# Kernel tuning notes

Hardware: AMD Instinct MI355X
Metric: run time of the kernel (lower is better)

## Reference

```python
import jax, jax.numpy as jnp
import numpy as np

N = 4096        # nodes (cells)
E = 131072      # edges (avg degree 32)
IN = 3000       # input features (genes)
HID = 128       # hidden dim per head
H = 4           # attention heads
LAT = 16        # latent dim
NEG_SLOPE = 0.2 # PyG GATConv leaky_relu slope


def _gat_sparse(x, src, dst, W, a_src, a_dst, b, concat):
    """PyG GATConv on an edge list (src -> dst, softmax grouped by dst)."""
    n = x.shape[0]
    h_, c = a_src.shape
    h = (x @ W).reshape(n, h_, c)                      # [N,H,C]
    e_src = (h * a_src[None]).sum(-1)                  # [N,H]
    e_dst = (h * a_dst[None]).sum(-1)                  # [N,H]
    e = jax.nn.leaky_relu(e_src[src] + e_dst[dst], NEG_SLOPE)  # [E,H]
    m = jax.ops.segment_max(e, dst, num_segments=n)
    ex = jnp.exp(e - m[dst])
    denom = jax.ops.segment_sum(ex, dst, num_segments=n)
    alpha = ex / (denom[dst] + 1e-16)                  # PyG softmax eps
    out = jax.ops.segment_sum(alpha[:, :, None] * h[src], dst, num_segments=n)
    out = out.reshape(n, h_ * c) if concat else out.mean(1)
    return out + b


def _gat_dense(x, W, a_src, a_dst, b, concat):
    """GATConv over the complete graph (the SVD low-rank reconstruction is
    generically fully dense, so to_sparse() keeps all N^2 entries; with
    used_edge_weight=False only the structure matters)."""
    n = x.shape[0]
    h_, c = a_src.shape
    h = (x @ W).reshape(n, h_, c)
    e_src = (h * a_src[None]).sum(-1)                  # [N,H]
    e_dst = (h * a_dst[None]).sum(-1)                  # [N,H]
    # scores[i (target), j (source), head]
    scores = jax.nn.leaky_relu(e_dst[:, None, :] + e_src[None, :, :], NEG_SLOPE)
    alpha = jax.nn.softmax(scores, axis=1)             # softmax over sources
    out = jnp.einsum('ijh,jhc->ihc', alpha, h)
    out = out.reshape(n, h_ * c) if concat else out.mean(1)
    return out + b


def setup_inputs() -> dict:
    key = jax.random.key(0)
    ks = jax.random.split(key, 16)
    s = 0.05
    x = jax.random.normal(ks[0], (N, IN), jnp.float32)
    src = jax.random.randint(ks[1], (E,), 0, N, jnp.int32)
    off = jax.random.randint(ks[2], (E,), 1, N, jnp.int32)
    dst = (src + off) % N                              # no self loops (PyG re-adds them)
    edge_index = jnp.stack([src, dst], axis=0)
    edge_attr = jax.random.uniform(ks[3], (E,), jnp.float32)
    D1 = H * HID
    return {
        'x': x, 'edge_index': edge_index, 'edge_attr': edge_attr,
        'W1': jax.random.normal(ks[4], (IN, D1), jnp.float32) * s,
        'a1_src': jax.random.normal(ks[5], (H, HID), jnp.float32) * s,
        'a1_dst': jax.random.normal(ks[6], (H, HID), jnp.float32) * s,
        'b1': jnp.zeros((D1,), jnp.float32),
        'Wm': jax.random.normal(ks[7], (D1, H * LAT), jnp.float32) * s,
        'am_src': jax.random.normal(ks[8], (H, LAT), jnp.float32) * s,
        'am_dst': jax.random.normal(ks[9], (H, LAT), jnp.float32) * s,
        'bm': jnp.zeros((LAT,), jnp.float32),
        'Ws': jax.random.normal(ks[10], (D1, H * LAT), jnp.float32) * s,
        'as_src': jax.random.normal(ks[11], (H, LAT), jnp.float32) * s,
        'as_dst': jax.random.normal(ks[12], (H, LAT), jnp.float32) * s,
        'bs': jnp.zeros((LAT,), jnp.float32),
    }


def reference(x, edge_index, edge_attr, W1, a1_src, a1_dst, b1,
              Wm, am_src, am_dst, bm, Ws, as_src, as_dst, bs):
    loops = jnp.arange(N, dtype=edge_index.dtype)
    src = jnp.concatenate([edge_index[0], loops])      # GATConv add_self_loops=True
    dst = jnp.concatenate([edge_index[1], loops])
    # branch 1: original sparse graph
    x1 = _gat_sparse(x, src, dst, W1, a1_src, a1_dst, b1, True)
    z_mean1 = _gat_sparse(x1, src, dst, Wm, am_src, am_dst, bm, False)
    z_log_std1 = _gat_sparse(x1, src, dst, Ws, as_src, as_dst, bs, False)
    # branch 2: SVD low-rank reconstructed adjacency => complete graph
    x2 = _gat_dense(x, W1, a1_src, a1_dst, b1, True)
    z_mean2 = _gat_dense(x2, Wm, am_src, am_dst, bm, False)
    z_log_std2 = _gat_dense(x2, Ws, as_src, as_dst, bs, False)
    return (z_mean1, z_log_std1, z_mean2, z_log_std2)
```

## Files before the change

kernel.cpp:

```cpp
#include <hip/hip_runtime.h>

typedef unsigned short u16;
typedef unsigned long long u64;
typedef __attribute__((ext_vector_type(8))) short short8;
typedef __attribute__((ext_vector_type(4))) float f32x4;

#define NN   4096
#define EE   131072
#define ETOT (EE + NN)
#define HH   4
#define IND  3000
#define KP   3008
#define D1   512
#define C1   128
#define C2   16

__device__ __forceinline__ float b2f(u16 u){
  union { unsigned int i; float f; } v; v.i = ((unsigned int)u) << 16; return v.f;
}
__device__ __forceinline__ u16 f2b(float f){
  unsigned int x = __float_as_uint(f);
  unsigned int r = (x + 0x7fffu + ((x >> 16) & 1u)) >> 16;
  return (u16)r;
}
__device__ __forceinline__ float lrelu(float x){ return x > 0.f ? x : 0.2f * x; }

__device__ __forceinline__ void glds16(const void* g, void* l){
  __builtin_amdgcn_global_load_lds(
      (const __attribute__((address_space(1))) unsigned int*)g,
      (__attribute__((address_space(3))) unsigned int*)l, 16, 0, 0);
}

__global__ void zero_out_kernel(float* p, int n){
  int i = blockIdx.x * blockDim.x + threadIdx.x;
  if (i < n) p[i] = 0.f;
}

__global__ __launch_bounds__(256) void cvtXW_kernel(const float* __restrict__ X,
    const float* __restrict__ W, u16* __restrict__ Xhi, u16* __restrict__ Xlo,
    u16* __restrict__ Whi, u16* __restrict__ Wlo){
  __shared__ float T[64][65];
  int b = blockIdx.x;
  if (b < 6016){
    int id = b * 256 + threadIdx.x;
    int m = id / 376, ch = id - m * 376;
    int k = ch * 8;
    float v[8];
    if (k + 8 <= IND){
      float4 a = *(const float4*)(X + (size_t)m * IND + k);
      float4 bb = *(const float4*)(X + (size_t)m * IND + k + 4);
      v[0]=a.x; v[1]=a.y; v[2]=a.z; v[3]=a.w; v[4]=bb.x; v[5]=bb.y; v[6]=bb.z; v[7]=bb.w;
    } else {
      #pragma unroll
      for (int j = 0; j < 8; ++j){ int kk = k + j; v[j] = (kk < IND) ? X[(size_t)m*IND + kk] : 0.f; }
    }
    u16 h8[8], l8[8];
    #pragma unroll
    for (int j = 0; j < 8; ++j){ h8[j] = f2b(v[j]); l8[j] = f2b(v[j] - b2f(h8[j])); }
    *(uint4*)(Xhi + (size_t)m * KP + k) = *(uint4*)h8;
    *(uint4*)(Xlo + (size_t)m * KP + k) = *(uint4*)l8;
  } else {
    int wb = b - 6016;
    int kb = wb % 47, nb = wb / 47;
    int k0 = kb * 64, n0 = nb * 64;
    int t = threadIdx.x;
    #pragma unroll
    for (int rr = 0; rr < 4; ++rr){
      int kl = (t >> 4) + rr * 16;
      int nn = (t & 15) * 4;
      int k = k0 + kl;
      float4 v = make_float4(0.f, 0.f, 0.f, 0.f);
      if (k < IND) v = *(const float4*)(W + (size_t)k * D1 + n0 + nn);
      T[kl][nn] = v.x; T[kl][nn+1] = v.y; T[kl][nn+2] = v.z; T[kl][nn+3] = v.w;
    }
    __syncthreads();
    int nloc = t >> 2, kseg = (t & 3) * 16;
    int n = n0 + nloc;
    #pragma unroll
    for (int c2 = 0; c2 < 2; ++c2){
      int kloc = kseg + c2 * 8;
      u16 h8[8], l8[8];
      #pragma unroll
      for (int j = 0; j < 8; ++j){
        float f = T[kloc + j][nloc];
        h8[j] = f2b(f); l8[j] = f2b(f - b2f(h8[j]));
      }
      *(uint4*)(Whi + (size_t)n * KP + k0 + kloc) = *(uint4*)h8;
      *(uint4*)(Wlo + (size_t)n * KP + k0 + kloc) = *(uint4*)l8;
    }
  }
}

__global__ __launch_bounds__(256) void cvtW2_kernel(const float* __restrict__ WM,
    const float* __restrict__ WS, u16* __restrict__ Wh, u16* __restrict__ Wl){
  __shared__ float T[64][65];
  int half = blockIdx.y;
  int k0 = blockIdx.x * 64;
  const float* W = half ? WS : WM;
  int t = threadIdx.x;
  #pragma unroll
  for (int p = 0; p < 4; ++p){
    int r = p * 16 + (t >> 4), c4 = (t & 15) * 4;
    float4 v = *(const float4*)(W + (size_t)(k0 + r) * 64 + c4);
    T[r][c4] = v.x; T[r][c4+1] = v.y; T[r][c4+2] = v.z; T[r][c4+3] = v.w;
  }
  __syncthreads();
  #pragma unroll
  for (int p = 0; p < 4; ++p){
    int n = p * 16 + (t >> 4), k4 = (t & 15) * 4;
    u16 h4[4], l4[4];
    #pragma unroll
    for (int j = 0; j < 4; ++j){
      float f = T[k4 + j][n];
      h4[j] = f2b(f); l4[j] = f2b(f - b2f(h4[j]));
    }
    size_t o = (size_t)(half * 64 + n) * 512 + k0 + k4;
    *(ushort4*)(Wh + o) = *(ushort4*)h4;
    *(ushort4*)(Wl + o) = *(ushort4*)l4;
  }
}

__global__ __launch_bounds__(512) void gemm_mfma(const u16* __restrict__ Xhi,
    const u16* __restrict__ Xlo, const u16* __restrict__ Whi, const u16* __restrict__ Wlo,
    float* __restrict__ Hh){
  __shared__ u16 sAh[64*64], sAl[64*64], sBh[64*64], sBl[64*64];
  int t = threadIdx.x, lane = t & 63;
  int wv = __builtin_amdgcn_readfirstlane(t >> 6);
  int wr = wv >> 1, wc = wv & 1;
  int bm = blockIdx.x * 64, bn = blockIdx.y * 64;
  f32x4 acc[2] = {};
  int srow = t >> 3;
  int sc = (t & 7) ^ (srow & 7);
  const char* gAh = (const char*)(Xhi + (size_t)(bm + srow) * KP) + sc * 16;
  const char* gAl = (const char*)(Xlo + (size_t)(bm + srow) * KP) + sc * 16;
  const char* gBh = (const char*)(Whi + (size_t)(bn + srow) * KP) + sc * 16;
  const char* gBl = (const char*)(Wlo + (size_t)(bn + srow) * KP) + sc * 16;
  char* lAh = (char*)sAh + t * 16;
  char* lAl = (char*)sAl + t * 16;
  char* lBh = (char*)sBh + t * 16;
  char* lBl = (char*)sBl + t * 16;
  int r16 = lane & 15, kq = lane >> 4;
  int arow = wr * 16 + r16;
  int brow0 = wc * 32 + r16;
  int brow1 = brow0 + 16;
  int aoff[2], b0off[2], b1off[2];
  #pragma unroll
  for (int ks = 0; ks < 2; ++ks){
    int cc = ks * 4 + kq;
    aoff[ks]  = arow  * 128 + ((cc ^ (arow  & 7)) * 16);
    b0off[ks] = brow0 * 128 + ((cc ^ (brow0 & 7)) * 16);
    b1off[ks] = brow1 * 128 + ((cc ^ (brow1 & 7)) * 16);
  }
  for (int kb = 0; kb < KP * 2; kb += 128){
    glds16(gAh + kb, lAh);
    glds16(gAl + kb, lAl);
    glds16(gBh + kb, lBh);
    glds16(gBl + kb, lBl);
    __syncthreads();
    #pragma unroll
    for (int ks = 0; ks < 2; ++ks){
      short8 ah = *(const short8*)((const char*)sAh + aoff[ks]);
      short8 al = *(const short8*)((const char*)sAl + aoff[ks]);
      short8 b0h = *(const short8*)((const char*)sBh + b0off[ks]);
      short8 b0l = *(const short8*)((const char*)sBl + b0off[ks]);
      short8 b1h = *(const short8*)((const char*)sBh + b1off[ks]);
      short8 b1l = *(const short8*)((const char*)sBl + b1off[ks]);
      acc[0] = __builtin_amdgcn_mfma_f32_16x16x32_bf16(ah, b0h, acc[0], 0, 0, 0);
      acc[0] = __builtin_amdgcn_mfma_f32_16x16x32_bf16(ah, b0l, acc[0], 0, 0, 0);
      acc[0] = __builtin_amdgcn_mfma_f32_16x16x32_bf16(al, b0h, acc[0], 0, 0, 0);
      acc[1] = __builtin_amdgcn_mfma_f32_16x16x32_bf16(ah, b1h, acc[1], 0, 0, 0);
      acc[1] = __builtin_amdgcn_mfma_f32_16x16x32_bf16(ah, b1l, acc[1], 0, 0, 0);
      acc[1] = __builtin_amdgcn_mfma_f32_16x16x32_bf16(al, b1h, acc[1], 0, 0, 0);
    }
    __syncthreads();
  }
  int cr = kq << 2, cc = r16;
  #pragma unroll
  for (int j = 0; j < 2; ++j){
    int row = bm + wr * 16 + cr;
    int col = bn + wc * 32 + j * 16 + cc;
    float* o = Hh + (size_t)row * D1 + col;
    #pragma unroll
    for (int r = 0; r < 4; ++r) o[(size_t)r * D1] = acc[j][r];
  }
}

__global__ __launch_bounds__(256) void gemm_h_split(const float* __restrict__ X,
    const float* __restrict__ Wc, float* __restrict__ Hh){
  __shared__ u16 Ahs[64][40], Als[64][40], Bhs[64][40], Bls[64][40];
  int t = threadIdx.x, lane = t & 63, wave = t >> 6;
  int wr = wave >> 1, wcc = wave & 1;
  int bm = blockIdx.x * 64, bn = blockIdx.y * 64;
  f32x4 acc[2][2] = {};
  int arow = t >> 2, akc = (t & 3) << 3;
  int brow = t >> 3, bnc = (t & 7) << 3;
  for (int k0 = 0; k0 < IND; k0 += 32){
    float va[8];
    size_t abase = (size_t)(bm + arow) * IND + k0 + akc;
    if (k0 + akc + 8 <= IND){
      float4 r0 = *(const float4*)(X + abase);
      float4 r1 = *(const float4*)(X + abase + 4);
      va[0]=r0.x; va[1]=r0.y; va[2]=r0.z; va[3]=r0.w;
      va[4]=r1.x; va[5]=r1.y; va[6]=r1.z; va[7]=r1.w;
    } else {
      #pragma unroll
      for (int j = 0; j < 8; ++j){
        int k = k0 + akc + j;
        va[j] = (k < IND) ? X[abase + j] : 0.f;
      }
    }
    #pragma unroll
    for (int j = 0; j < 8; ++j){
      u16 hb = f2b(va[j]);
      Ahs[arow][akc + j] = hb;
      Als[arow][akc + j] = f2b(va[j] - b2f(hb));
    }
    {
      int gk = k0 + brow;
      float vb[8];
      if (gk < IND){
        const float* wp = Wc + (size_t)gk * D1 + bn + bnc;
        float4 r0 = *(const float4*)wp;
        float4 r1 = *(const float4*)(wp + 4);
        vb[0]=r0.x; vb[1]=r0.y; vb[2]=r0.z; vb[3]=r0.w;
        vb[4]=r1.x; vb[5]=r1.y; vb[6]=r1.z; vb[7]=r1.w;
      } else {
        #pragma unroll
        for (int j = 0; j < 8; ++j) vb[j] = 0.f;
      }
      #pragma unroll
      for (int j = 0; j < 8; ++j){
        u16 hb = f2b(vb[j]);
        Bhs[bnc + j][brow] = hb;
        Bls[bnc + j][brow] = f2b(vb[j] - b2f(hb));
      }
    }
    __syncthreads();
    int r16 = lane & 15, kq = (lane >> 4) << 3;
    short8 a0h = *(const short8*)&Ahs[wr*32      + r16][kq];
    short8 a1h = *(const short8*)&Ahs[wr*32 + 16 + r16][kq];
    short8 a0l = *(const short8*)&Als[wr*32      + r16][kq];
    short8 a1l = *(const short8*)&Als[wr*32 + 16 + r16][kq];
    short8 b0h = *(const short8*)&Bhs[wcc*32      + r16][kq];
    short8 b1h = *(const short8*)&Bhs[wcc*32 + 16 + r16][kq];
    short8 b0l = *(const short8*)&Bls[wcc*32      + r16][kq];
    short8 b1l = *(const short8*)&Bls[wcc*32 + 16 + r16][kq];
    acc[0][0] = __builtin_amdgcn_mfma_f32_16x16x32_bf16(a0h, b0h, acc[0][0], 0, 0, 0);
    acc[0][1] = __builtin_amdgcn_mfma_f32_16x16x32_bf16(a0h, b1h, acc[0][1], 0, 0, 0);
    acc[1][0] = __builtin_amdgcn_mfma_f32_16x16x32_bf16(a1h, b0h, acc[1][0], 0, 0, 0);
    acc[1][1] = __builtin_amdgcn_mfma_f32_16x16x32_bf16(a1h, b1h, acc[1][1], 0, 0, 0);
    acc[0][0] = __builtin_amdgcn_mfma_f32_16x16x32_bf16(a0h, b0l, acc[0][0], 0, 0, 0);
    acc[0][1] = __builtin_amdgcn_mfma_f32_16x16x32_bf16(a0h, b1l, acc[0][1], 0, 0, 0);
    acc[1][0] = __builtin_amdgcn_mfma_f32_16x16x32_bf16(a1h, b0l, acc[1][0], 0, 0, 0);
    acc[1][1] = __builtin_amdgcn_mfma_f32_16x16x32_bf16(a1h, b1l, acc[1][1], 0, 0, 0);
    acc[0][0] = __builtin_amdgcn_mfma_f32_16x16x32_bf16(a0l, b0h, acc[0][0], 0, 0, 0);
    acc[0][1] = __builtin_amdgcn_mfma_f32_16x16x32_bf16(a0l, b1h, acc[0][1], 0, 0, 0);
    acc[1][0] = __builtin_amdgcn_mfma_f32_16x16x32_bf16(a1l, b0h, acc[1][0], 0, 0, 0);
    acc[1][1] = __builtin_amdgcn_mfma_f32_16x16x32_bf16(a1l, b1h, acc[1][1], 0, 0, 0);
    __syncthreads();
  }
  int cr = (lane >> 4) << 2, cc = lane & 15;
  for (int i = 0; i < 2; ++i) for (int j = 0; j < 2; ++j){
    int row = bm + wr*32 + i*16 + cr;
    int col = bn + wcc*32 + j*16 + cc;
    float* o = Hh + (size_t)row * D1 + col;
    for (int r = 0; r < 4; ++r) o[(size_t)r * D1] = acc[i][j][r];
  }
}

__global__ __launch_bounds__(256) void transpose_h(const float* __restrict__ h,
    float* __restrict__ hT, u16* __restrict__ h16){
  __shared__ float T[64][65];
  int bm = blockIdx.x * 64, bc = blockIdx.y * 64;
  int t = threadIdx.x;
  #pragma unroll
  for (int p = 0; p < 4; ++p){
    int r = p * 16 + (t >> 4), c4 = (t & 15) * 4;
    float4 v = *(const float4*)(h + (size_t)(bm + r) * D1 + bc + c4);
    T[r][c4] = v.x; T[r][c4+1] = v.y; T[r][c4+2] = v.z; T[r][c4+3] = v.w;
    u16 q[4] = { f2b(v.x), f2b(v.y), f2b(v.z), f2b(v.w) };
    *(ushort4*)(h16 + (size_t)(bm + r) * D1 + bc + c4) = *(ushort4*)q;
  }
  __syncthreads();
  #pragma unroll
  for (int p = 0; p < 4; ++p){
    int c = p * 16 + (t >> 4), m4 = (t & 15) * 4;
    float4 o = make_float4(T[m4][c], T[m4+1][c], T[m4+2][c], T[m4+3][c]);
    *(float4*)(hT + (size_t)(bc + c) * NN + bm + m4) = o;
  }
}

__global__ __launch_bounds__(256) void evec128(const float* __restrict__ hsrc,
    const float* __restrict__ as_, const float* __restrict__ ad_,
    float* __restrict__ es, float* __restrict__ ed){
  int idx = blockIdx.x * 256 + threadIdx.x;
  if (idx >= NN * HH) return;
  int h = idx & 3;
  const float4* hp = (const float4*)(hsrc + (size_t)idx * C1);
  const float4* ap = (const float4*)(as_ + h * C1);
  const float4* dp = (const float4*)(ad_ + h * C1);
  float s1 = 0.f, s2 = 0.f;
  #pragma unroll
  for (int c = 0; c < 32; ++c){
    float4 v = hp[c], a = ap[c], d = dp[c];
    s1 += v.x*a.x + v.y*a.y + v.z*a.z + v.w*a.w;
    s2 += v.x*d.x + v.y*d.y + v.z*d.z + v.w*d.w;
  }
  es[idx] = s1; ed[idx] = s2;
}

__global__ void zero_kernel(int* p, int n){
  int i = blockIdx.x * blockDim.x + threadIdx.x;
  if (i < n) p[i] = 0;
}
__global__ void hist_kernel(const int* __restrict__ dstA, int* __restrict__ deg){
  int e = blockIdx.x * blockDim.x + threadIdx.x;
  if (e < ETOT){
    int d = (e < EE) ? dstA[e] : (e - EE);
    atomicAdd(&deg[d & (NN-1)], 1);
  }
}
__global__ __launch_bounds__(1024) void scan_kernel(const int* __restrict__ deg,
    int* __restrict__ off, int* __restrict__ cur){
  __shared__ int wsum[16];
  int t = threadIdx.x, lane = t & 63, wv = t >> 6;
  int v0 = deg[t*4], v1 = deg[t*4+1], v2 = deg[t*4+2], v3 = deg[t*4+3];
  int s = v0 + v1 + v2 + v3;
  int sc = s;
  #pragma unroll
  for (int o = 1; o < 64; o <<= 1){
    int y = __shfl_up(sc, o);
    if (lane >= o) sc += y;
  }
  if (lane == 63) wsum[wv] = sc;
  __syncthreads();
  int base = 0;
  #pragma unroll
  for (int i = 0; i < 16; ++i) base += (i < wv) ? wsum[i] : 0;
  int excl = base + sc - s;
  int a0 = excl, a1 = a0 + v0, a2 = a1 + v1, a3 = a2 + v2;
  off[t*4] = a0; off[t*4+1] = a1; off[t*4+2] = a2; off[t*4+3] = a3;
  cur[t*4] = a0; cur[t*4+1] = a1; cur[t*4+2] = a2; cur[t*4+3] = a3;
  if (t == 1023) off[4096] = base + sc;
}
__global__ void scatter_kernel(const int* __restrict__ srcA, const int* __restrict__ dstA,
    int* __restrict__ cur, int* __restrict__ sidx){
  int e = blockIdx.x * blockDim.x + threadIdx.x;
  if (e < ETOT){
    int s, d;
    if (e < EE){ s = srcA[e]; d = dstA[e]; } else { s = d = e - EE; }
    int pos = atomicAdd(&cur[d & (NN-1)], 1);
    pos = min(max(pos, 0), ETOT - 1);
    sidx[pos] = s & (NN-1);
  }
}

__global__ __launch_bounds__(256) void sparse1(const u16* __restrict__ h16,
    const float* __restrict__ es, const float* __restrict__ ed,
    const int* __restrict__ off, const int* __restrict__ sidx,
    const float* __restrict__ bias, u16* __restrict__ x1h, u16* __restrict__ x1l){
  int n = blockIdx.x, t = threadIdx.x, w = t >> 6;
// ... 294 lines not shown
    }
  } else {
    if (t < NC){
      int h = t / C, c = t % C;
      size_t base = (size_t)h * (NN + 1);
      float p1N = P1[(base + NN)    * Cp + c];
      float p1k = P1[(base + Kh[h]) * Cp + c];
      float p2k = P2[(base + Kh[h]) * Cp + c];
      vals[t] = (Ed[h] * (p1N - p1k) + E2d[h] * p2k) / Den[h];
    }
    __syncthreads();
    if (t < C){
      float z = (vals[t] + vals[C + t] + vals[2*C + t] + vals[3*C + t]) * 0.25f + bias[t];
      outF[(size_t)i * C + t] = z;
    }
  }
}

__global__ __launch_bounds__(256) void dense_out1(const float* __restrict__ P1,
    const float* __restrict__ P2, const float* __restrict__ usort,
    const float* __restrict__ ed, const float* __restrict__ bias,
    u16* __restrict__ outH, u16* __restrict__ outL){
  dense_body<C1, false>(P1, P2, usort, ed, bias, nullptr, outH, outL, blockIdx.x);
}

struct Dn2 { const float* P1[2]; const float* P2[2]; const float* us[2];
             const float* ed[2]; const float* bias[2]; float* out[2]; };
__global__ __launch_bounds__(256) void dense_out2(Dn2 a){
  int s = blockIdx.y;
  dense_body<C2, true>(a.P1[s], a.P2[s], a.us[s], a.ed[s], a.bias[s], a.out[s],
                       nullptr, nullptr, blockIdx.x);
}

extern "C" void kernel_launch(void* const* d_in, const int* in_sizes, int n_in,
                              void* d_out, int out_size, void* d_ws, size_t ws_size,
                              hipStream_t stream){
  const float* X   = (const float*)d_in[0];
  const int*   EI  = (const int*)d_in[1];
  const float* W1  = (const float*)d_in[3];
  const float* A1S = (const float*)d_in[4];
  const float* A1D = (const float*)d_in[5];
  const float* B1  = (const float*)d_in[6];
  const float* WM  = (const float*)d_in[7];
  const float* AMS = (const float*)d_in[8];
  const float* AMD = (const float*)d_in[9];
  const float* BM  = (const float*)d_in[10];
  const float* WS  = (const float*)d_in[11];
  const float* ASS = (const float*)d_in[12];
  const float* ASD = (const float*)d_in[13];
  const float* BS  = (const float*)d_in[14];
  float* OUT = (float*)d_out;
  (void)in_sizes; (void)n_in;

  if (ws_size < (size_t)56 * 1024 * 1024){
    zero_out_kernel<<<dim3((out_size + 255)/256), 256, 0, stream>>>(OUT, out_size);
    return;
  }
  bool fast = (ws_size >= (size_t)68 * 1024 * 1024);

  const size_t MB = 1024 * 1024;
  char* w = (char*)d_ws;
  size_t o = 0;
  auto alloc = [&](size_t bytes) -> void* {
    void* p = w + o;
    o += (bytes + 255) & ~(size_t)255;
    return p;
  };
  int*   deg  = (int*)  alloc(NN * 4);
  int*   coff = (int*)  alloc((NN + 1) * 4);
  int*   cur  = (int*)  alloc(NN * 4);
  int*   sidx = (int*)  alloc((size_t)ETOT * 4);
  float* e1s  = (float*)alloc(NN * HH * 4);
  float* e1d  = (float*)alloc(NN * HH * 4);
  float* us1  = (float*)alloc(HH * NN * 4);
  int*   pm1  = (int*)  alloc(HH * NN * 4);
  float* em1s = (float*)alloc(NN * HH * 4);
  float* em1d = (float*)alloc(NN * HH * 4);
  float* es1s = (float*)alloc(NN * HH * 4);
  float* es1d = (float*)alloc(NN * HH * 4);
  float* em2s = (float*)alloc(NN * HH * 4);
  float* em2d = (float*)alloc(NN * HH * 4);
  float* es2s = (float*)alloc(NN * HH * 4);
  float* es2d = (float*)alloc(NN * HH * 4);
  float* us2m = (float*)alloc(HH * NN * 4);
  int*   pm2m = (int*)  alloc(HH * NN * 4);
  float* us2s = (float*)alloc(HH * NN * 4);
  int*   pm2s = (int*)  alloc(HH * NN * 4);
  u16*   Wh2  = (u16*)  alloc(128 * 512 * 2);
  u16*   Wl2  = (u16*)  alloc(128 * 512 * 2);
  float* h    = (float*)alloc((size_t)NN * D1 * 4);
  char*  BIG  = w + o;
  size_t szX = (size_t)NN * KP * 2, szW = (size_t)D1 * KP * 2;
  u16* Xhi = (u16*)BIG;
  u16* Xlo = (u16*)(BIG + szX);
  u16* Whi = (u16*)(BIG + 2*szX);
  u16* Wlo = (u16*)(BIG + 2*szX + szW);
  u16*   x1h = (u16*)  (BIG + 0*MB);
  u16*   x1l = (u16*)  (BIG + 4*MB);
  u16*   x2h = (u16*)  (BIG + 8*MB);
  u16*   x2l = (u16*)  (BIG + 12*MB);
  float* hT  = (float*)(BIG + 16*MB);
  u16*   h16 = (u16*)  (BIG + 24*MB);
  float* P1a = (float*)(BIG + 28*MB);
  float* P2a = (float*)(BIG + 37*MB);
  float* hm1  = (float*)(BIG + 16*MB);
  float* hs1  = (float*)(BIG + 17*MB);
  float* hm2T = (float*)(BIG + 18*MB);
  float* hs2T = (float*)(BIG + 19*MB);
  float* P1m  = (float*)(BIG + 20*MB);
  float* P2m  = (float*)(BIG + 21*MB + 512*1024);
  float* P1s  = (float*)(BIG + 23*MB);
  float* P2s  = (float*)(BIG + 24*MB + 512*1024);

  const int* srcA = EI;
  const int* dstA = EI + EE;

  cvtW2_kernel<<<dim3(8, 2), 256, 0, stream>>>(WM, WS, Wh2, Wl2);
  if (fast){
    cvtXW_kernel<<<dim3(6016 + 47*8), 256, 0, stream>>>(X, W1, Xhi, Xlo, Whi, Wlo);
    gemm_mfma<<<dim3(NN/64, D1/64), 512, 0, stream>>>(Xhi, Xlo, Whi, Wlo, h);
  } else {
    gemm_h_split<<<dim3(NN/64, D1/64), 256, 0, stream>>>(X, W1, h);
  }
  transpose_h<<<dim3(NN/64, D1/64), 256, 0, stream>>>(h, hT, h16);
  evec128<<<dim3(NN*HH/256), 256, 0, stream>>>(h, A1S, A1D, e1s, e1d);
  zero_kernel<<<dim3(16), 256, 0, stream>>>(deg, NN);
  hist_kernel<<<dim3((ETOT + 255)/256), 256, 0, stream>>>(dstA, deg);
  scan_kernel<<<dim3(1), 1024, 0, stream>>>(deg, coff, cur);
  scatter_kernel<<<dim3((ETOT + 255)/256), 256, 0, stream>>>(srcA, dstA, cur, sidx);
  sparse1<<<dim3(NN), 256, 0, stream>>>(h16, e1s, e1d, coff, sidx, B1, x1h, x1l);
  {
    RkA ra; ra.in[0] = e1s; ra.in[1] = e1s; ra.us[0] = us1; ra.us[1] = us1;
    ra.pm[0] = pm1; ra.pm[1] = pm1;
    rank_kernel<<<dim3(64, 4), 1024, 0, stream>>>(ra);
    PfxA pa; pa.T[0] = hT; pa.T[1] = hT; pa.pm[0] = pm1; pa.pm[1] = pm1;
    pa.us[0] = us1; pa.us[1] = us1; pa.P1[0] = P1a; pa.P1[1] = P1a;
    pa.P2[0] = P2a; pa.P2[1] = P2a;
    prefix_kernel<<<dim3(HH*(C1+1), 1), 512, 0, stream>>>(pa, C1);
    dense_out1<<<dim3(NN), 256, 0, stream>>>(P1a, P2a, us1, e1d, B1, x2h, x2l);
  }
  {
    GsA ga;
    ga.x1h = x1h; ga.x1l = x1l; ga.x2h = x2h; ga.x2l = x2l;
    ga.Wh = Wh2; ga.Wl = Wl2;
    ga.hm1 = hm1; ga.hs1 = hs1; ga.hm2T = hm2T; ga.hs2T = hs2T;
    ga.AMS = AMS; ga.AMD = AMD; ga.ASS = ASS; ga.ASD = ASD;
    ga.em1s = em1s; ga.em1d = em1d; ga.es1s = es1s; ga.es1d = es1d;
    ga.em2s = em2s; ga.em2d = em2d; ga.es2s = es2s; ga.es2d = es2d;
    gemm_small_fused<<<dim3(NN/32, 2), 256, 0, stream>>>(ga);
  }
  {
    Sp2 sp;
    sp.h[0] = hm1; sp.h[1] = hs1; sp.es[0] = em1s; sp.es[1] = es1s;
    sp.ed[0] = em1d; sp.ed[1] = es1d; sp.bias[0] = BM; sp.bias[1] = BS;
    sp.out[0] = OUT; sp.out[1] = OUT + (size_t)NN*C2;
    sparse2<<<dim3(NN, 2), 64, 0, stream>>>(sp, coff, sidx);
  }
  {
    RkA ra; ra.in[0] = em2s; ra.in[1] = es2s; ra.us[0] = us2m; ra.us[1] = us2s;
    ra.pm[0] = pm2m; ra.pm[1] = pm2s;
    rank_kernel<<<dim3(64, 8), 1024, 0, stream>>>(ra);
    PfxA pa; pa.T[0] = hm2T; pa.T[1] = hs2T; pa.pm[0] = pm2m; pa.pm[1] = pm2s;
    pa.us[0] = us2m; pa.us[1] = us2s; pa.P1[0] = P1m; pa.P1[1] = P1s;
    pa.P2[0] = P2m; pa.P2[1] = P2s;
    prefix_kernel<<<dim3(HH*(C2+1), 2), 512, 0, stream>>>(pa, C2);
    Dn2 dn;
    dn.P1[0] = P1m; dn.P1[1] = P1s; dn.P2[0] = P2m; dn.P2[1] = P2s;
    dn.us[0] = us2m; dn.us[1] = us2s; dn.ed[0] = em2d; dn.ed[1] = es2d;
    dn.bias[0] = BM; dn.bias[1] = BS;
    dn.out[0] = OUT + (size_t)2*NN*C2; dn.out[1] = OUT + (size_t)3*NN*C2;
    dense_out2<<<dim3(NN, 2), 256, 0, stream>>>(dn);
  }
}
```

Baseline: 386.3 us.

## Fuse X bf16 split into split-K 128x128 MFMA GEMM and fold reduction into transpose

Removes the separate X conversion pass and instead converts fp32 X to hi/lo bf16 inside the GEMM's LDS staging, using truncation. The GEMM moves to 128x128 tiles with 32x32x16 MFMAs and a 4-way split-K over 512 blocks, writing partial results that the transpose kernel sums. The transpose kernel also computes the attention score vectors, which removes the evec128 kernel. The goal is to avoid writing and re-reading the large bf16 copy of X and to get more reuse per tile. In exchange it adds split-K partial traffic of about 32MB, and truncating instead of rounding for the hi part slightly changes the numerics.

Measured after the change: 409.0 us. 5.9% more time.

```diff
diff --git a/kernel.cpp b/kernel.cpp
--- a/kernel.cpp
+++ b/kernel.cpp
@@ -4,13 +4,16 @@
 typedef unsigned long long u64;
 typedef __attribute__((ext_vector_type(8))) short short8;
 typedef __attribute__((ext_vector_type(4))) float f32x4;
+typedef __attribute__((ext_vector_type(16))) float f32x16;
 
 #define NN   4096
 #define EE   131072
 #define ETOT (EE + NN)
 #define HH   4
 #define IND  3000
-#define KP   3008
+#define KP   3072
+#define KSP  4
+#define KPER 768
 #define D1   512
 #define C1   128
 #define C2   16
@@ -36,58 +39,36 @@
   if (i < n) p[i] = 0.f;
 }
 
-__global__ __launch_bounds__(256) void cvtXW_kernel(const float* __restrict__ X,
-    const float* __restrict__ W, u16* __restrict__ Xhi, u16* __restrict__ Xlo,
+__global__ __launch_bounds__(256) void cvtW1_kernel(const float* __restrict__ W,
     u16* __restrict__ Whi, u16* __restrict__ Wlo){
   __shared__ float T[64][65];
-  int b = blockIdx.x;
-  if (b < 6016){
-    int id = b * 256 + threadIdx.x;
-    int m = id / 376, ch = id - m * 376;
-    int k = ch * 8;
-    float v[8];
-    if (k + 8 <= IND){
-      float4 a = *(const float4*)(X + (size_t)m * IND + k);
-      float4 bb = *(const float4*)(X + (size_t)m * IND + k + 4);
-      v[0]=a.x; v[1]=a.y; v[2]=a.z; v[3]=a.w; v[4]=bb.x; v[5]=bb.y; v[6]=bb.z; v[7]=bb.w;
-    } else {
-      #pragma unroll
-      for (int j = 0; j < 8; ++j){ int kk = k + j; v[j] = (kk < IND) ? X[(size_t)m*IND + kk] : 0.f; }
-    }
+  int wb = blockIdx.x;
+  int kb = wb % 48, nbb = wb / 48;
+  int k0 = kb * 64, n0 = nbb * 64;
+  int t = threadIdx.x;
+  #pragma unroll
+  for (int rr = 0; rr < 4; ++rr){
+    int kl = (t >> 4) + rr * 16;
+    int nn2 = (t & 15) * 4;
+    int k = k0 + kl;
+    float4 v = make_float4(0.f, 0.f, 0.f, 0.f);
+    if (k < IND) v = *(const float4*)(W + (size_t)k * D1 + n0 + nn2);
+    T[kl][nn2] = v.x; T[kl][nn2+1] = v.y; T[kl][nn2+2] = v.z; T[kl][nn2+3] = v.w;
+  }
+  __syncthreads();
+  int nloc = t >> 2, kseg = (t & 3) * 16;
+  int n = n0 + nloc;
+  #pragma unroll
+  for (int c2 = 0; c2 < 2; ++c2){
+    int kloc = kseg + c2 * 8;
     u16 h8[8], l8[8];
     #pragma unroll
-    for (int j = 0; j < 8; ++j){ h8[j] = f2b(v[j]); l8[j] = f2b(v[j] - b2f(h8[j])); }
-    *(uint4*)(Xhi + (size_t)m * KP + k) = *(uint4*)h8;
-    *(uint4*)(Xlo + (size_t)m * KP + k) = *(uint4*)l8;
-  } else {
-    int wb = b - 6016;
-    int kb = wb % 47, nb = wb / 47;
-    int k0 = kb * 64, n0 = nb * 64;
-    int t = threadIdx.x;
-    #pragma unroll
-    for (int rr = 0; rr < 4; ++rr){
-      int kl = (t >> 4) + rr * 16;
-      int nn = (t & 15) * 4;
-      int k = k0 + kl;
-      float4 v = make_float4(0.f, 0.f, 0.f, 0.f);
-      if (k < IND) v = *(const float4*)(W + (size_t)k * D1 + n0 + nn);
-      T[kl][nn] = v.x; T[kl][nn+1] = v.y; T[kl][nn+2] = v.z; T[kl][nn+3] = v.w;
-    }
-    __syncthreads();
-    int nloc = t >> 2, kseg = (t & 3) * 16;
-    int n = n0 + nloc;
-    #pragma unroll
-    for (int c2 = 0; c2 < 2; ++c2){
-      int kloc = kseg + c2 * 8;
-      u16 h8[8], l8[8];
-      #pragma unroll
-      for (int j = 0; j < 8; ++j){
-        float f = T[kloc + j][nloc];
-        h8[j] = f2b(f); l8[j] = f2b(f - b2f(h8[j]));
-      }
-      *(uint4*)(Whi + (size_t)n * KP + k0 + kloc) = *(uint4*)h8;
-      *(uint4*)(Wlo + (size_t)n * KP + k0 + kloc) = *(uint4*)l8;
-    }
+    for (int j = 0; j < 8; ++j){
+      float f = T[kloc + j][nloc];
+      h8[j] = f2b(f); l8[j] = f2b(f - b2f(h8[j]));
+    }
+    *(uint4*)(Whi + (size_t)n * KP + k0 + kloc) = *(uint4*)h8;
+    *(uint4*)(Wlo + (size_t)n * KP + k0 + kloc) = *(uint4*)l8;
   }
 }
 
@@ -120,193 +101,174 @@
   }
 }
 
-__global__ __launch_bounds__(512) void gemm_mfma(const u16* __restrict__ Xhi,
-    const u16* __restrict__ Xlo, const u16* __restrict__ Whi, const u16* __restrict__ Wlo,
-    float* __restrict__ Hh){
-  __shared__ u16 sAh[64*64], sAl[64*64], sBh[64*64], sBl[64*64];
+__global__ __launch_bounds__(256, 2) void gemm_mfma3(const float* __restrict__ X,
+    const u16* __restrict__ Whi, const u16* __restrict__ Wlo,
+    float* __restrict__ HP){
+  __shared__ u16 sAh[128*64], sAl[128*64], sBh[128*64], sBl[128*64];
   int t = threadIdx.x, lane = t & 63;
   int wv = __builtin_amdgcn_readfirstlane(t >> 6);
   int wr = wv >> 1, wc = wv & 1;
-  int bm = blockIdx.x * 64, bn = blockIdx.y * 64;
-  f32x4 acc[2] = {};
-  int srow = t >> 3;
-  int sc = (t & 7) ^ (srow & 7);
-  const char* gAh = (const char*)(Xhi + (size_t)(bm + srow) * KP) + sc * 16;
-  const char* gAl = (const char*)(Xlo + (size_t)(bm + srow) * KP) + sc * 16;
-  const char* gBh = (const char*)(Whi + (size_t)(bn + srow) * KP) + sc * 16;
-  const char* gBl = (const char*)(Wlo + (size_t)(bn + srow) * KP) + sc * 16;
-  char* lAh = (char*)sAh + t * 16;
-  char* lAl = (char*)sAl + t * 16;
-  char* lBh = (char*)sBh + t * 16;
-  char* lBl = (char*)sBl + t * 16;
-  int r16 = lane & 15, kq = lane >> 4;
-  int arow = wr * 16 + r16;
-  int brow0 = wc * 32 + r16;
-  int brow1 = brow0 + 16;
-  int aoff[2], b0off[2], b1off[2];
-  #pragma unroll
-  for (int ks = 0; ks < 2; ++ks){
-    int cc = ks * 4 + kq;
-    aoff[ks]  = arow  * 128 + ((cc ^ (arow  & 7)) * 16);
-    b0off[ks] = brow0 * 128 + ((cc ^ (brow0 & 7)) * 16);
-    b1off[ks] = brow1 * 128 + ((cc ^ (brow1 & 7)) * 16);
-  }
-  for (int kb = 0; kb < KP * 2; kb += 128){
-    glds16(gAh + kb, lAh);
-    glds16(gAl + kb, lAl);
-    glds16(gBh + kb, lBh);
-    glds16(gBl + kb, lBl);
+  int bid = blockIdx.x;
+  int lid = (bid & 7) * 64 + (bid >> 3);
+  int nb = lid & 3;
+  int g  = lid >> 2;
+  int kp = g & 3, mb = g >> 2;
+  int bm = mb * 128, bn = nb * 128;
+  int k0 = kp * KPER;
+
+  f32x16 acc[2][2] = {};
+
+  int arow = t >> 1, ahalf = t & 1;
+  const float* gA = X + (size_t)(bm + arow) * IND + k0 + ahalf * 32;
+  char* aw_h[4]; char* aw_l[4];
+  #pragma unroll
+  for (int j2 = 0; j2 < 4; ++j2){
+    int c = ahalf * 4 + j2;
+    int cs = c ^ (arow & 7);
+    aw_h[j2] = (char*)sAh + arow * 128 + cs * 16;
+    aw_l[j2] = (char*)sAl + arow * 128 + cs * 16;
+  }
+  const char* gB[8]; char* lB[8];
+  #pragma unroll
+  for (int q = 0; q < 8; ++q){
+    int s = (q & 3) * 256 + t;
+    int br = s >> 3, bc = (s & 7) ^ (br & 7);
+    const u16* base = (q < 4) ? Whi : Wlo;
+    gB[q] = (const char*)(base + (size_t)(bn + br) * KP + k0) + bc * 16;
+    lB[q] = (char*)((q < 4) ? sBh : sBl) + s * 16;
+  }
+  int l31 = lane & 31, lhi = lane >> 5;
+  int aoff[2][4], boff[2][4];
+  #pragma unroll
+  for (int m = 0; m < 2; ++m)
+    #pragma unroll
+    for (int ks = 0; ks < 4; ++ks){
+      int row = wr * 64 + m * 32 + l31;
+      int cb = 2 * ks + lhi;
+      aoff[m][ks] = row * 128 + ((cb ^ (row & 7)) * 16);
+    }
+  #pragma unroll
+  for (int n = 0; n < 2; ++n)
+    #pragma unroll
+    for (int ks = 0; ks < 4; ++ks){
+      int row = wc * 64 + n * 32 + l31;
+      int cb = 2 * ks + lhi;
+      boff[n][ks] = row * 128 + ((cb ^ (row & 7)) * 16);
+    }
+
+  for (int kb = 0; kb < KPER; kb += 64){
+    int kbase = k0 + kb + ahalf * 32;
+    float4 va[8];
+    const float* gk = gA + kb;
+    #pragma unroll
+    for (int j = 0; j < 8; ++j){
+      va[j] = (kbase + j * 4 < IND) ? *(const float4*)(gk + j * 4)
+                                    : make_float4(0.f, 0.f, 0.f, 0.f);
+    }
+    #pragma unroll
+    for (int j2 = 0; j2 < 4; ++j2){
+      float e[8] = { va[2*j2].x, va[2*j2].y, va[2*j2].z, va[2*j2].w,
+                     va[2*j2+1].x, va[2*j2+1].y, va[2*j2+1].z, va[2*j2+1].w };
+      unsigned hh8[4], ll8[4];
+      #pragma unroll
+      for (int p = 0; p < 4; ++p){
+        unsigned x0 = __float_as_uint(e[2*p]);
+        unsigned x1 = __float_as_uint(e[2*p+1]);
+        hh8[p] = (x0 >> 16) | (x1 & 0xffff0000u);
+        float l0 = e[2*p]   - __uint_as_float(x0 & 0xffff0000u);
+        float l1 = e[2*p+1] - __uint_as_float(x1 & 0xffff0000u);
+        ll8[p] = (__float_as_uint(l0) >> 16) | (__float_as_uint(l1) & 0xffff0000u);
+      }
+      *(uint4*)aw_h[j2] = *(uint4*)hh8;
+      *(uint4*)aw_l[j2] = *(uint4*)ll8;
+    }
+    #pragma unroll
+    for (int q = 0; q < 8; ++q) glds16(gB[q] + kb * 2, lB[q]);
     __syncthreads();
     #pragma unroll
-    for (int ks = 0; ks < 2; ++ks){
-      short8 ah = *(const short8*)((const char*)sAh + aoff[ks]);
-      short8 al = *(const short8*)((const char*)sAl + aoff[ks]);
-      short8 b0h = *(const short8*)((const char*)sBh + b0off[ks]);
-      short8 b0l = *(const short8*)((const char*)sBl + b0off[ks]);
-      short8 b1h = *(const short8*)((const char*)sBh + b1off[ks]);
-      short8 b1l = *(const short8*)((const char*)sBl + b1off[ks]);
-      acc[0] = __builtin_amdgcn_mfma_f32_16x16x32_bf16(ah, b0h, acc[0], 0, 0, 0);
-      acc[0] = __builtin_amdgcn_mfma_f32_16x16x32_bf16(ah, b0l, acc[0], 0, 0, 0);
-      acc[0] = __builtin_amdgcn_mfma_f32_16x16x32_bf16(al, b0h, acc[0], 0, 0, 0);
-      acc[1] = __builtin_amdgcn_mfma_f32_16x16x32_bf16(ah, b1h, acc[1], 0, 0, 0);
-      acc[1] = __builtin_amdgcn_mfma_f32_16x16x32_bf16(ah, b1l, acc[1], 0, 0, 0);
-      acc[1] = __builtin_amdgcn_mfma_f32_16x16x32_bf16(al, b1h, acc[1], 0, 0, 0);
+    for (int ks = 0; ks < 4; ++ks){
+      short8 ah[2], al[2], bh[2], bl[2];
+      #pragma unroll
+      for (int m = 0; m < 2; ++m){
+        ah[m] = *(const short8*)((const char*)sAh + aoff[m][ks]);
+        al[m] = *(const short8*)((const char*)sAl + aoff[m][ks]);
+      }
+      #pragma unroll
+      for (int n = 0; n < 2; ++n){
+        bh[n] = *(const short8*)((const char*)sBh + boff[n][ks]);
+        bl[n] = *(const short8*)((const char*)sBl + boff[n][ks]);
+      }
+      #pragma unroll
+      for (int m = 0; m < 2; ++m)
+        #pragma unroll
+        for (int n = 0; n < 2; ++n){
+          acc[m][n] = __builtin_amdgcn_mfma_f32_32x32x16_bf16(ah[m], bh[n], acc[m][n], 0, 0, 0);
+          acc[m][n] = __builtin_amdgcn_mfma_f32_32x32x16_bf16(ah[m], bl[n], acc[m][n], 0, 0, 0);
+          acc[m][n] = __builtin_amdgcn_mfma_f32_32x32x16_bf16(al[m], bh[n], acc[m][n], 0, 0, 0);
+        }
     }
     __syncthreads();
   }
-  int cr = kq << 2, cc = r16;
-  #pragma unroll
-  for (int j = 0; j < 2; ++j){
-    int row = bm + wr * 16 + cr;
-    int col = bn + wc * 32 + j * 16 + cc;
-    float* o = Hh + (size_t)row * D1 + col;
-    #pragma unroll
-    for (int r = 0; r < 4; ++r) o[(size_t)r * D1] = acc[j][r];
-  }
-}
-
-__global__ __launch_bounds__(256) void gemm_h_split(const float* __restrict__ X,
-    const float* __restrict__ Wc, float* __restrict__ Hh){
-  __shared__ u16 Ahs[64][40], Als[64][40], Bhs[64][40], Bls[64][40];
-  int t = threadIdx.x, lane = t & 63, wave = t >> 6;
-  int wr = wave >> 1, wcc = wave & 1;
-  int bm = blockIdx.x * 64, bn = blockIdx.y * 64;
-  f32x4 acc[2][2] = {};
-  int arow = t >> 2, akc = (t & 3) << 3;
-  int brow = t >> 3, bnc = (t & 7) << 3;
-  for (int k0 = 0; k0 < IND; k0 += 32){
-    float va[8];
-    size_t abase = (size_t)(bm + arow) * IND + k0 + akc;
-    if (k0 + akc + 8 <= IND){
-      float4 r0 = *(const float4*)(X + abase);
-      float4 r1 = *(const float4*)(X + abase + 4);
-      va[0]=r0.x; va[1]=r0.y; va[2]=r0.z; va[3]=r0.w;
-      va[4]=r1.x; va[5]=r1.y; va[6]=r1.z; va[7]=r1.w;
-    } else {
-      #pragma unroll
-      for (int j = 0; j < 8; ++j){
-        int k = k0 + akc + j;
-        va[j] = (k < IND) ? X[abase + j] : 0.f;
+  float* hp = HP + (size_t)kp * ((size_t)NN * D1);
+  #pragma unroll
+  for (int m = 0; m < 2; ++m)
+    #pragma unroll
+    for (int n = 0; n < 2; ++n){
+      int row0 = bm + wr * 64 + m * 32 + 4 * lhi;
+      int col  = bn + wc * 64 + n * 32 + l31;
+      #pragma unroll
+      for (int r = 0; r < 16; ++r){
+        int row = row0 + (r & 3) + 8 * (r >> 2);
+        hp[(size_t)row * D1 + col] = acc[m][n][r];
       }
     }
-    #pragma unroll
-    for (int j = 0; j < 8; ++j){
-      u16 hb = f2b(va[j]);
-      Ahs[arow][akc + j] = hb;
-      Als[arow][akc + j] = f2b(va[j] - b2f(hb));
-    }
-    {
-      int gk = k0 + brow;
-      float vb[8];
-      if (gk < IND){
-        const float* wp = Wc + (size_t)gk * D1 + bn + bnc;
-        float4 r0 = *(const float4*)wp;
-        float4 r1 = *(const float4*)(wp + 4);
-        vb[0]=r0.x; vb[1]=r0.y; vb[2]=r0.z; vb[3]=r0.w;
-        vb[4]=r1.x; vb[5]=r1.y; vb[6]=r1.z; vb[7]=r1.w;
-      } else {
-        #pragma unroll
-        for (int j = 0; j < 8; ++j) vb[j] = 0.f;
-      }
-      #pragma unroll
-      for (int j = 0; j < 8; ++j){
-        u16 hb = f2b(vb[j]);
-        Bhs[bnc + j][brow] = hb;
-        Bls[bnc + j][brow] = f2b(vb[j] - b2f(hb));
-      }
-    }
-    __syncthreads();
-    int r16 = lane & 15, kq = (lane >> 4) << 3;
-    short8 a0h = *(const short8*)&Ahs[wr*32      + r16][kq];
-    short8 a1h = *(const short8*)&Ahs[wr*32 + 16 + r16][kq];
-    short8 a0l = *(const short8*)&Als[wr*32      + r16][kq];
-    short8 a1l = *(const short8*)&Als[wr*32 + 16 + r16][kq];
-    short8 b0h = *(const short8*)&Bhs[wcc*32      + r16][kq];
-    short8 b1h = *(const short8*)&Bhs[wcc*32 + 16 + r16][kq];
-    short8 b0l = *(const short8*)&Bls[wcc*32      + r16][kq];
-    short8 b1l = *(const short8*)&Bls[wcc*32 + 16 + r16][kq];
-    acc[0][0] = __builtin_amdgcn_mfma_f32_16x16x32_bf16(a0h, b0h, acc[0][0], 0, 0, 0);
-    acc[0][1] = __builtin_amdgcn_mfma_f32_16x16x32_bf16(a0h, b1h, acc[0][1], 0, 0, 0);
-    acc[1][0] = __builtin_amdgcn_mfma_f32_16x16x32_bf16(a1h, b0h, acc[1][0], 0, 0, 0);
-    acc[1][1] = __builtin_amdgcn_mfma_f32_16x16x32_bf16(a1h, b1h, acc[1][1], 0, 0, 0);
-    acc[0][0] = __builtin_amdgcn_mfma_f32_16x16x32_bf16(a0h, b0l, acc[0][0], 0, 0, 0);
-    acc[0][1] = __builtin_amdgcn_mfma_f32_16x16x32_bf16(a0h, b1l, acc[0][1], 0, 0, 0);
-    acc[1][0] = __builtin_amdgcn_mfma_f32_16x16x32_bf16(a1h, b0l, acc[1][0], 0, 0, 0);
-    acc[1][1] = __builtin_amdgcn_mfma_f32_16x16x32_bf16(a1h, b1l, acc[1][1], 0, 0, 0);
-    acc[0][0] = __builtin_amdgcn_mfma_f32_16x16x32_bf16(a0l, b0h, acc[0][0], 0, 0, 0);
-    acc[0][1] = __builtin_amdgcn_mfma_f32_16x16x32_bf16(a0l, b1h, acc[0][1], 0, 0, 0);
-    acc[1][0] = __builtin_amdgcn_mfma_f32_16x16x32_bf16(a1l, b0h, acc[1][0], 0, 0, 0);
-    acc[1][1] = __builtin_amdgcn_mfma_f32_16x16x32_bf16(a1l, b1h, acc[1][1], 0, 0, 0);
-    __syncthreads();
-  }
-  int cr = (lane >> 4) << 2, cc = lane & 15;
-  for (int i = 0; i < 2; ++i) for (int j = 0; j < 2; ++j){
-    int row = bm + wr*32 + i*16 + cr;
-    int col = bn + wcc*32 + j*16 + cc;
-    float* o = Hh + (size_t)row * D1 + col;
-    for (int r = 0; r < 4; ++r) o[(size_t)r * D1] = acc[i][j][r];
-  }
-}
-
-__global__ __launch_bounds__(256) void transpose_h(const float* __restrict__ h,
-    float* __restrict__ hT, u16* __restrict__ h16){
-  __shared__ float T[64][65];
-  int bm = blockIdx.x * 64, bc = blockIdx.y * 64;
+}
+
+__global__ __launch_bounds__(256) void transpose_h_red(const float* __restrict__ HP,
+    float* __restrict__ hT, u16* __restrict__ h16,
+    const float* __restrict__ A1S, const float* __restrict__ A1D,
+    float* __restrict__ es, float* __restrict__ ed){
+  __shared__ float T[64][129];
+  __shared__ float R1[64][4], R2[64][4];
+  int bm = blockIdx.x * 64;
+  int hh = blockIdx.y;
+  int bc = hh * 128;
   int t = threadIdx.x;
-  #pragma unroll
-  for (int p = 0; p < 4; ++p){
-    int r = p * 16 + (t >> 4), c4 = (t & 15) * 4;
-    float4 v = *(const float4*)(h + (size_t)(bm + r) * D1 + bc + c4);
-    T[r][c4] = v.x; T[r][c4+1] = v.y; T[r][c4+2] = v.z; T[r][c4+3] = v.w;
-    u16 q[4] = { f2b(v.x), f2b(v.y), f2b(v.z), f2b(v.w) };
-    *(ushort4*)(h16 + (size_t)(bm + r) * D1 + bc + c4) = *(ushort4*)q;
-  }
-  __syncthreads();
-  #pragma unroll
-  for (int p = 0; p < 4; ++p){
-    int c = p * 16 + (t >> 4), m4 = (t & 15) * 4;
+  int r = t >> 2, c0 = (t & 3) * 32;
+  const size_t NND1 = (size_t)NN * D1;
+  float s1 = 0.f, s2 = 0.f;
+  #pragma unroll
+  for (int j = 0; j < 8; ++j){
+    int c = c0 + j * 4;
+    size_t off = (size_t)(bm + r) * D1 + bc + c;
+    float4 v = *(const float4*)(HP + off);
+    #pragma unroll
+    for (int p = 1; p < 4; ++p){
+      float4 u = *(const float4*)(HP + (size_t)p * NND1 + off);
+      v.x += u.x; v.y += u.y; v.z += u.z; v.w += u.w;
+    }
+    T[r][c] = v.x; T[r][c+1] = v.y; T[r][c+2] = v.z; T[r][c+3] = v.w;
+    u16 q4[4] = { f2b(v.x), f2b(v.y), f2b(v.z), f2b(v.w) };
+    *(ushort4*)(h16 + off) = *(ushort4*)q4;
+    int cb = bc + c;
+    s1 = fmaf(v.x, A1S[cb], fmaf(v.y, A1S[cb+1], fmaf(v.z, A1S[cb+2], fmaf(v.w, A1S[cb+3], s1))));
+    s2 = fmaf(v.x, A1D[cb], fmaf(v.y, A1D[cb+1], fmaf(v.z, A1D[cb+2], fmaf(v.w, A1D[cb+3], s2))));
+  }
+  R1[r][t & 3] = s1; R2[r][t & 3] = s2;
+  __syncthreads();
+  if (t < 64){
+    float v1 = R1[t][0] + R1[t][1] + R1[t][2] + R1[t][3];
+    float v2 = R2[t][0] + R2[t][1] + R2[t][2] + R2[t][3];
+    es[(bm + t) * HH + hh] = v1;
+    ed[(bm + t) * HH + hh] = v2;
+  }
+  int c = t >> 1, m0 = (t & 1) * 32;
+  #pragma unroll
+  for (int j = 0; j < 8; ++j){
+    int m4 = m0 + j * 4;
     float4 o = make_float4(T[m4][c], T[m4+1][c], T[m4+2][c], T[m4+3][c]);
     *(float4*)(hT + (size_t)(bc + c) * NN + bm + m4) = o;
   }
-}
-
-__global__ __launch_bounds__(256) void evec128(const float* __restrict__ hsrc,
-    const float* __restrict__ as_, const float* __restrict__ ad_,
-    float* __restrict__ es, float* __restrict__ ed){
-  int idx = blockIdx.x * 256 + threadIdx.x;
-  if (idx >= NN * HH) return;
-  int h = idx & 3;
-  const float4* hp = (const float4*)(hsrc + (size_t)idx * C1);
-  const float4* ap = (const float4*)(as_ + h * C1);
-  const float4* dp = (const float4*)(ad_ + h * C1);
-  float s1 = 0.f, s2 = 0.f;
-  #pragma unroll
-  for (int c = 0; c < 32; ++c){
-    float4 v = hp[c], a = ap[c], d = dp[c];
-    s1 += v.x*a.x + v.y*a.y + v.z*a.z + v.w*a.w;
-    s2 += v.x*d.x + v.y*d.y + v.z*d.z + v.w*d.w;
-  }
-  es[idx] = s1; ed[idx] = s2;
 }
 
 __global__ void zero_kernel(int* p, int n){
@@ -707,11 +669,10 @@
   float* OUT = (float*)d_out;
   (void)in_sizes; (void)n_in;
 
-  if (ws_size < (size_t)56 * 1024 * 1024){
+  if (ws_size < (size_t)64 * 1024 * 1024){
     zero_out_kernel<<<dim3((out_size + 255)/256), 256, 0, stream>>>(OUT, out_size);
     return;
   }
-  bool fast = (ws_size >= (size_t)68 * 1024 * 1024);
 
   const size_t MB = 1024 * 1024;
   char* w = (char*)d_ws;
@@ -743,13 +704,10 @@
   int*   pm2s = (int*)  alloc(HH * NN * 4);
   u16*   Wh2  = (u16*)  alloc(128 * 512 * 2);
   u16*   Wl2  = (u16*)  alloc(128 * 512 * 2);
-  float* h    = (float*)alloc((size_t)NN * D1 * 4);
   char*  BIG  = w + o;
-  size_t szX = (size_t)NN * KP * 2, szW = (size_t)D1 * KP * 2;
-  u16* Xhi = (u16*)BIG;
-  u16* Xlo = (u16*)(BIG + szX);
-  u16* Whi = (u16*)(BIG + 2*szX);
-  u16* Wlo = (u16*)(BIG + 2*szX + szW);
+  u16*   WhiB = (u16*)(BIG + 0);
+  u16*   WloB = (u16*)(BIG + (size_t)3200*1024);
+  float* hp   = (float*)(BIG + 28*MB);
   u16*   x1h = (u16*)  (BIG + 0*MB);
   u16*   x1l = (u16*)  (BIG + 4*MB);
   u16*   x2h = (u16*)  (BIG + 8*MB);
@@ -770,15 +728,10 @@
   const int* srcA = EI;
   const int* dstA = EI + EE;
 
+  cvtW1_kernel<<<dim3(48*8), 256, 0, stream>>>(W1, WhiB, WloB);
   cvtW2_kernel<<<dim3(8, 2), 256, 0, stream>>>(WM, WS, Wh2, Wl2);
-  if (fast){
-    cvtXW_kernel<<<dim3(6016 + 47*8), 256, 0, stream>>>(X, W1, Xhi, Xlo, Whi, Wlo);
-    gemm_mfma<<<dim3(NN/64, D1/64), 512, 0, stream>>>(Xhi, Xlo, Whi, Wlo, h);
-  } else {
-    gemm_h_split<<<dim3(NN/64, D1/64), 256, 0, stream>>>(X, W1, h);
-  }
-  transpose_h<<<dim3(NN/64, D1/64), 256, 0, stream>>>(h, hT, h16);
-  evec128<<<dim3(NN*HH/256), 256, 0, stream>>>(h, A1S, A1D, e1s, e1d);
+  gemm_mfma3<<<dim3(512), 256, 0, stream>>>(X, WhiB, WloB, hp);
+  transpose_h_red<<<dim3(64, 4), 256, 0, stream>>>(hp, hT, h16, A1S, A1D, e1s, e1d);
   zero_kernel<<<dim3(16), 256, 0, stream>>>(deg, NN);
   hist_kernel<<<dim3((ETOT + 255)/256), 256, 0, stream>>>(dstA, deg);
   scan_kernel<<<dim3(1), 1024, 0, stream>>>(deg, coff, cur);
```

## Double-buffer MFMA GEMM with 64x128 tiles and remapped block order

Applied to the files above, without the earlier changes.

Reworks the split-bf16 MFMA GEMM for h = X@W1. Each block now computes a 64x128 output tile with 8 waves each owning a 32x32 sub-tile, so every LDS fragment load feeds more MFMAs. LDS staging is double-buffered so the next K-slice loads while the current one computes, which drops one barrier per iteration. A 1D grid of 256 blocks with a swizzled block-id mapping is meant to improve L2 reuse. LDS use and accumulator registers go up, and with only 256 blocks occupancy and tail balance change.

New measurement: 411.1 us. 6.4% more time.

```diff
diff --git a/kernel.cpp b/kernel.cpp
--- a/kernel.cpp
+++ b/kernel.cpp
@@ -123,66 +123,100 @@
 __global__ __launch_bounds__(512) void gemm_mfma(const u16* __restrict__ Xhi,
     const u16* __restrict__ Xlo, const u16* __restrict__ Whi, const u16* __restrict__ Wlo,
     float* __restrict__ Hh){
-  __shared__ u16 sAh[64*64], sAl[64*64], sBh[64*64], sBl[64*64];
+  __shared__ u16 sAh[2][64*64], sAl[2][64*64];
+  __shared__ u16 sBh[2][128*64], sBl[2][128*64];
   int t = threadIdx.x, lane = t & 63;
   int wv = __builtin_amdgcn_readfirstlane(t >> 6);
-  int wr = wv >> 1, wc = wv & 1;
-  int bm = blockIdx.x * 64, bn = blockIdx.y * 64;
-  f32x4 acc[2] = {};
+  int wr = wv >> 2, wc = wv & 3;
+  int bid = blockIdx.x;
+  int lid = (bid & 7) * 32 + (bid >> 3);
+  int mb = lid >> 2, nb = lid & 3;
+  int bm = mb * 64, bn = nb * 128;
+  f32x4 acc[2][2] = {};
   int srow = t >> 3;
   int sc = (t & 7) ^ (srow & 7);
   const char* gAh = (const char*)(Xhi + (size_t)(bm + srow) * KP) + sc * 16;
   const char* gAl = (const char*)(Xlo + (size_t)(bm + srow) * KP) + sc * 16;
-  const char* gBh = (const char*)(Whi + (size_t)(bn + srow) * KP) + sc * 16;
-  const char* gBl = (const char*)(Wlo + (size_t)(bn + srow) * KP) + sc * 16;
-  char* lAh = (char*)sAh + t * 16;
-  char* lAl = (char*)sAl + t * 16;
-  char* lBh = (char*)sBh + t * 16;
-  char* lBl = (char*)sBl + t * 16;
+  int s1 = 512 + t;
+  int br0 = t >> 3,  bc0 = (t & 7) ^ (br0 & 7);
+  int br1 = s1 >> 3, bc1 = (s1 & 7) ^ (br1 & 7);
+  const char* gBh0 = (const char*)(Whi + (size_t)(bn + br0) * KP) + bc0 * 16;
+  const char* gBl0 = (const char*)(Wlo + (size_t)(bn + br0) * KP) + bc0 * 16;
+  const char* gBh1 = (const char*)(Whi + (size_t)(bn + br1) * KP) + bc1 * 16;
+  const char* gBl1 = (const char*)(Wlo + (size_t)(bn + br1) * KP) + bc1 * 16;
   int r16 = lane & 15, kq = lane >> 4;
-  int arow = wr * 16 + r16;
-  int brow0 = wc * 32 + r16;
-  int brow1 = brow0 + 16;
-  int aoff[2], b0off[2], b1off[2];
-  #pragma unroll
-  for (int ks = 0; ks < 2; ++ks){
-    int cc = ks * 4 + kq;
-    aoff[ks]  = arow  * 128 + ((cc ^ (arow  & 7)) * 16);
-    b0off[ks] = brow0 * 128 + ((cc ^ (brow0 & 7)) * 16);
-    b1off[ks] = brow1 * 128 + ((cc ^ (brow1 & 7)) * 16);
-  }
-  for (int kb = 0; kb < KP * 2; kb += 128){
-    glds16(gAh + kb, lAh);
-    glds16(gAl + kb, lAl);
-    glds16(gBh + kb, lBh);
-    glds16(gBl + kb, lBl);
+  int aoff[2][2], boff[2][2];
+  #pragma unroll
+  for (int m = 0; m < 2; ++m)
+    #pragma unroll
+    for (int ks = 0; ks < 2; ++ks){
+      int arow = wr * 32 + m * 16 + r16;
+      int cc = ks * 4 + kq;
+      aoff[m][ks] = arow * 128 + ((cc ^ (arow & 7)) * 16);
+    }
+  #pragma unroll
+  for (int n = 0; n < 2; ++n)
+    #pragma unroll
+    for (int ks = 0; ks < 2; ++ks){
+      int brow = wc * 32 + n * 16 + r16;
+      int cc = ks * 4 + kq;
+      boff[n][ks] = brow * 128 + ((cc ^ (brow & 7)) * 16);
+    }
+
+  #define STAGE(i, b) do {                                  \
+    int ko = (i) * 128;                                     \
+    glds16(gAh + ko, (char*)sAh[b] + t * 16);               \
+    glds16(gAl + ko, (char*)sAl[b] + t * 16);               \
+    glds16(gBh0 + ko, (char*)sBh[b] + t * 16);              \
+    glds16(gBh1 + ko, (char*)sBh[b] + s1 * 16);             \
+    glds16(gBl0 + ko, (char*)sBl[b] + t * 16);              \
+    glds16(gBl1 + ko, (char*)sBl[b] + s1 * 16);             \
+  } while (0)
+
+  STAGE(0, 0);
+  __syncthreads();
+  for (int i = 0; i < 47; ++i){
+    int cur = i & 1;
+    if (i < 46) STAGE(i + 1, cur ^ 1);
+    const char* pAh = (const char*)sAh[cur];
+    const char* pAl = (const char*)sAl[cur];
+    const char* pBh = (const char*)sBh[cur];
+    const char* pBl = (const char*)sBl[cur];
+    #pragma unroll
+    for (int ks = 0; ks < 2; ++ks){
+      short8 ah[2], al[2], bh[2], bl[2];
+      #pragma unroll
+      for (int m = 0; m < 2; ++m){
+        ah[m] = *(const short8*)(pAh + aoff[m][ks]);
+        al[m] = *(const short8*)(pAl + aoff[m][ks]);
+      }
+      #pragma unroll
+      for (int n = 0; n < 2; ++n){
+        bh[n] = *(const short8*)(pBh + boff[n][ks]);
+        bl[n] = *(const short8*)(pBl + boff[n][ks]);
+      }
+      #pragma unroll
+      for (int m = 0; m < 2; ++m)
+        #pragma unroll
+        for (int n = 0; n < 2; ++n){
+          acc[m][n] = __builtin_amdgcn_mfma_f32_16x16x32_bf16(ah[m], bh[n], acc[m][n], 0, 0, 0);
+          acc[m][n] = __builtin_amdgcn_mfma_f32_16x16x32_bf16(ah[m], bl[n], acc[m][n], 0, 0, 0);
+          acc[m][n] = __builtin_amdgcn_mfma_f32_16x16x32_bf16(al[m], bh[n], acc[m][n], 0, 0, 0);
+        }
+    }
     __syncthreads();
-    #pragma unroll
-    for (int ks = 0; ks < 2; ++ks){
-      short8 ah = *(const short8*)((const char*)sAh + aoff[ks]);
-      short8 al = *(const short8*)((const char*)sAl + aoff[ks]);
-      short8 b0h = *(const short8*)((const char*)sBh + b0off[ks]);
-      short8 b0l = *(const short8*)((const char*)sBl + b0off[ks]);
-      short8 b1h = *(const short8*)((const char*)sBh + b1off[ks]);
-      short8 b1l = *(const short8*)((const char*)sBl + b1off[ks]);
-      acc[0] = __builtin_amdgcn_mfma_f32_16x16x32_bf16(ah, b0h, acc[0], 0, 0, 0);
-      acc[0] = __builtin_amdgcn_mfma_f32_16x16x32_bf16(ah, b0l, acc[0], 0, 0, 0);
-      acc[0] = __builtin_amdgcn_mfma_f32_16x16x32_bf16(al, b0h, acc[0], 0, 0, 0);
-      acc[1] = __builtin_amdgcn_mfma_f32_16x16x32_bf16(ah, b1h, acc[1], 0, 0, 0);
-      acc[1] = __builtin_amdgcn_mfma_f32_16x16x32_bf16(ah, b1l, acc[1], 0, 0, 0);
-      acc[1] = __builtin_amdgcn_mfma_f32_16x16x32_bf16(al, b1h, acc[1], 0, 0, 0);
-    }
-    __syncthreads();
-  }
-  int cr = kq << 2, cc = r16;
-  #pragma unroll
-  for (int j = 0; j < 2; ++j){
-    int row = bm + wr * 16 + cr;
-    int col = bn + wc * 32 + j * 16 + cc;
-    float* o = Hh + (size_t)row * D1 + col;
-    #pragma unroll
-    for (int r = 0; r < 4; ++r) o[(size_t)r * D1] = acc[j][r];
-  }
+  }
+  #undef STAGE
+  #pragma unroll
+  for (int m = 0; m < 2; ++m)
+    #pragma unroll
+    for (int n = 0; n < 2; ++n){
+      int row = bm + wr * 32 + m * 16 + kq * 4;
+      int col = bn + wc * 32 + n * 16 + r16;
+      float* o = Hh + (size_t)row * D1 + col;
+      #pragma unroll
+      for (int r = 0; r < 4; ++r) o[(size_t)r * D1] = acc[m][n][r];
+    }
 }
 
 __global__ __launch_bounds__(256) void gemm_h_split(const float* __restrict__ X,
@@ -773,7 +807,7 @@
   cvtW2_kernel<<<dim3(8, 2), 256, 0, stream>>>(WM, WS, Wh2, Wl2);
   if (fast){
     cvtXW_kernel<<<dim3(6016 + 47*8), 256, 0, stream>>>(X, W1, Xhi, Xlo, Whi, Wlo);
-    gemm_mfma<<<dim3(NN/64, D1/64), 512, 0, stream>>>(Xhi, Xlo, Whi, Wlo, h);
+    gemm_mfma<<<dim3(256), 512, 0, stream>>>(Xhi, Xlo, Whi, Wlo, h);
   } else {
     gemm_h_split<<<dim3(NN/64, D1/64), 256, 0, stream>>>(X, W1, h);
   }
```
